# Kernel tuning notes

Hardware: AMD Instinct MI355X
Metric: run time of the kernel (lower is better)

Reference implementation:

```python
import jax, jax.numpy as jnp
import numpy as np

B, L, E, F = 4096, 200, 128, 64
NU = NI = 100000

def setup_inputs() -> dict:
    key = jax.random.key(0)
    ks = jax.random.split(key, 8)
    return {
        "user_ids": jax.random.randint(ks[0], (B,), 0, NU),
        "item_ids": jax.random.randint(ks[1], (B, L), 0, NI),
        "features": jax.random.normal(ks[2], (B, L, F), dtype=jnp.float32),
        "user_emb": jax.random.normal(ks[3], (NU, E), dtype=jnp.float32) * 0.1,
        "item_emb": jax.random.normal(ks[4], (NI, E), dtype=jnp.float32) * 0.1,
        "feat_w1": jax.random.normal(ks[5], (E, E + F), dtype=jnp.float32) * (2.0 / (E + F)) ** 0.5,
        "feat_b1": jnp.zeros((E,), jnp.float32),
        "feat_w2": jax.random.normal(ks[6], (E, E), dtype=jnp.float32) * (2.0 / E) ** 0.5,
        "feat_b2": jnp.zeros((E,), jnp.float32),
        "w1": jax.random.normal(ks[7], (E, 3 * E), dtype=jnp.float32) * (2.0 / (3 * E)) ** 0.5,
        "b1": jnp.zeros((E,), jnp.float32),
        "w2": jax.random.normal(jax.random.fold_in(key, 99), (1, E), dtype=jnp.float32) * (2.0 / E) ** 0.5,
        "b2": jnp.zeros((1,), jnp.float32),
    }

def reference(user_ids, item_ids, features, user_emb, item_emb,
              feat_w1, feat_b1, feat_w2, feat_b2, w1, b1, w2, b2):
    user = user_emb[user_ids]                      # [B, E]
    items = item_emb[item_ids]                     # [B, L, E]
    usern = jnp.broadcast_to(user[:, None, :], items.shape)  # [B, L, E]
    # FeatureNet: concat(user, features) -> Linear -> relu -> Linear -> relu
    fx = jnp.concatenate([usern, features], axis=-1)           # [B, L, E+F]
    fx = jax.nn.relu(jnp.einsum('blf,ef->ble', fx, feat_w1) + feat_b1)
    comp = jax.nn.relu(jnp.einsum('ble,oe->blo', fx, feat_w2) + feat_b2)  # [B, L, E]
    # attention MLP over concat(user, item, comp)
    x = jnp.concatenate([usern, items, comp], axis=-1)         # [B, L, 3E]
    x = jax.nn.relu(jnp.einsum('blf,ef->ble', x, w1) + b1)
    logits = jnp.einsum('ble,oe->blo', x, w2) + b2             # [B, L, 1]
    attn = jax.nn.softmax(logits, axis=1)                      # softmax over items
    out = user + jnp.sum(items * attn, axis=1)                 # [B, E]
    return out
```

## Files before the change

kernel.cpp:

```cpp
#include <hip/hip_runtime.h>
#include <math.h>

#define BB 4096
#define LL 200
#define EE 128
#define FF 64
#define NTHREADS 512

#define CROWS 32
#define NCH 7

#define PITCH_F  72
#define PITCH_FX 136
#define PITCH_X3 264

typedef __attribute__((ext_vector_type(4))) float  floatx4;
typedef __attribute__((ext_vector_type(8))) short  shortx8;

#define MFMA16(a, b, c) __builtin_amdgcn_mfma_f32_16x16x32_bf16((a), (b), (c), 0, 0, 0)

__device__ __forceinline__ unsigned cvt_pk_bf16(float lo, float hi) {
    unsigned r;
    asm("v_cvt_pk_bf16_f32 %0, %1, %2" : "=v"(r) : "v"(lo), "v"(hi));
    return r;
}
__device__ __forceinline__ unsigned short f2bf(float f) {
    return (unsigned short)cvt_pk_bf16(f, f);
}
__device__ __forceinline__ uint2 pk4(float4 v) {
    uint2 o;
    o.x = cvt_pk_bf16(v.x, v.y);
    o.y = cvt_pk_bf16(v.z, v.w);
    return o;
}

__device__ __forceinline__ shortx8 load_bfrag(const float* p) {
    float4 v0 = ((const float4*)p)[0];
    float4 v1 = ((const float4*)p)[1];
    union { unsigned u[4]; shortx8 s; } r;
    r.u[0] = cvt_pk_bf16(v0.x, v0.y);
    r.u[1] = cvt_pk_bf16(v0.z, v0.w);
    r.u[2] = cvt_pk_bf16(v1.x, v1.y);
    r.u[3] = cvt_pk_bf16(v1.z, v1.w);
    return r.s;
}

__device__ __forceinline__ float waveMax(float v) {
    #pragma unroll
    for (int off = 32; off > 0; off >>= 1)
        v = fmaxf(v, __shfl_xor(v, off, 64));
    return v;
}
__device__ __forceinline__ float waveSum(float v) {
    #pragma unroll
    for (int off = 32; off > 0; off >>= 1)
        v += __shfl_xor(v, off, 64);
    return v;
}

__global__ __launch_bounds__(NTHREADS, 4)
void usernet_mfma(const int* __restrict__ user_ids,
                  const int* __restrict__ item_ids,
                  const float* __restrict__ features,
                  const float* __restrict__ user_emb,
                  const float* __restrict__ item_emb,
                  const float* __restrict__ feat_w1,
                  const float* __restrict__ feat_b1,
                  const float* __restrict__ feat_w2,
                  const float* __restrict__ feat_b2,
                  const float* __restrict__ w1,
                  const float* __restrict__ b1,
                  const float* __restrict__ w2,
                  const float* __restrict__ b2,
                  float* __restrict__ out)
{
    __shared__ __align__(16) unsigned short s_feat[CROWS * PITCH_F];
    __shared__ __align__(16) unsigned short s_fx  [CROWS * PITCH_FX];
    __shared__ __align__(16) unsigned short s_x3  [CROWS * PITCH_X3];
    __shared__ float s_user[EE];
    __shared__ float s_bias1[EE];
    __shared__ float s_bias2[EE];
    __shared__ float s_bias3[EE];
    __shared__ float s_w2[EE];
    __shared__ float s_lp[8][CROWS];
    __shared__ float s_logit[208];
    __shared__ float s_attn[208];
    __shared__ float s_red[12];
    __shared__ float s_part[4][EE];

    const int b    = blockIdx.x;
    const int tid  = threadIdx.x;
    const int lane = tid & 63;
    const int wv   = tid >> 6;
    const int m    = lane & 15;
    const int q    = lane >> 4;
    const int n0   = wv * 16 + m;

    shortx8 B1[2];
    shortx8 B2[4];
    shortx8 B3[8];
    #pragma unroll
    for (int ks = 0; ks < 2; ++ks)
        B1[ks] = load_bfrag(feat_w1 + (size_t)n0 * (EE + FF) + EE + ks * 32 + q * 8);
    #pragma unroll
    for (int ks = 0; ks < 4; ++ks)
        B2[ks] = load_bfrag(feat_w2 + (size_t)n0 * EE + ks * 32 + q * 8);
    #pragma unroll
    for (int ks = 0; ks < 8; ++ks)
        B3[ks] = load_bfrag(w1 + (size_t)n0 * (3 * EE) + EE + ks * 32 + q * 8);

    if (tid < 32) {
        const int uid = user_ids[b];
        ((float4*)s_user)[tid] = ((const float4*)(user_emb + (size_t)uid * EE))[tid];
    }
    if (tid >= 64 && tid < 64 + EE) {
        s_bias2[tid - 64] = feat_b2[tid - 64];
        s_w2[tid - 64]    = w2[tid - 64];
    }
    __syncthreads();

    if (tid < 256) {
        const int e    = tid & (EE - 1);
        const int half = tid >> 7;
        const float* wrow = half ? (w1 + (size_t)e * (3 * EE))
                                 : (feat_w1 + (size_t)e * (EE + FF));
        float acc = 0.f;
        #pragma unroll 8
        for (int k = 0; k < EE; ++k) acc += wrow[k] * s_user[k];
        if (half == 0) s_bias1[e] = acc + feat_b1[e];
        else           s_bias3[e] = acc + b1[e];
    }
    __syncthreads();

    const float bias1_0 = s_bias1[n0];
    const float bias2_0 = s_bias2[n0];
    const float bias3_0 = s_bias3[n0];
    const float w2_0    = s_w2[n0];

    for (int ch = 0; ch < NCH; ++ch) {
        const int row0 = ch * CROWS;
        const int ntl  = (ch < NCH - 1) ? 2 : 1;
        const int rows = ntl * 16;

        if (ch > 0 && tid < CROWS) {
            float p = 0.f;
            #pragma unroll
            for (int w = 0; w < 8; ++w) p += s_lp[w][tid];
            s_logit[row0 - CROWS + tid] = p;
        }

        for (int idx = tid; idx < rows * 16; idx += NTHREADS) {
            const int r = idx >> 4, c4 = idx & 15;
            const int l = row0 + r;
            float4 v = make_float4(0.f, 0.f, 0.f, 0.f);
            if (l < LL) v = ((const float4*)features)[((size_t)b * LL + l) * 16 + c4];
            *(uint2*)&s_feat[r * PITCH_F + c4 * 4] = pk4(v);
        }
        for (int idx = tid; idx < rows * 32; idx += NTHREADS) {
            const int r = idx >> 5, c4 = idx & 31;
            const int l = row0 + r;
            float4 v = make_float4(0.f, 0.f, 0.f, 0.f);
            if (l < LL) {
                const int id = item_ids[(size_t)b * LL + l];
                v = ((const float4*)item_emb)[(size_t)id * 32 + c4];
            }
            *(uint2*)&s_x3[r * PITCH_X3 + c4 * 4] = pk4(v);
        }
        __syncthreads();

        for (int mt = 0; mt < ntl; ++mt) {
            floatx4 a0 = {0.f, 0.f, 0.f, 0.f};
            const unsigned short* ap = s_feat + (mt * 16 + m) * PITCH_F + q * 8;
            #pragma unroll
            for (int ks = 0; ks < 2; ++ks) {
                shortx8 af = *(const shortx8*)(ap + ks * 32);
                a0 = MFMA16(af, B1[ks], a0);
            }
            #pragma unroll
            for (int r = 0; r < 4; ++r) {
                const int row = mt * 16 + q * 4 + r;
                float v0 = a0[r] + bias1_0; v0 = v0 > 0.f ? v0 : 0.f;
                s_fx[row * PITCH_FX + n0] = f2bf(v0);
            }
        }
        __syncthreads();

        for (int mt = 0; mt < ntl; ++mt) {
            floatx4 a0 = {0.f, 0.f, 0.f, 0.f};
            const unsigned short* ap = s_fx + (mt * 16 + m) * PITCH_FX + q * 8;
            #pragma unroll
            for (int ks = 0; ks < 4; ++ks) {
                shortx8 af = *(const shortx8*)(ap + ks * 32);
                a0 = MFMA16(af, B2[ks], a0);
            }
            #pragma unroll
            for (int r = 0; r < 4; ++r) {
                const int row = mt * 16 + q * 4 + r;
                float v0 = a0[r] + bias2_0; v0 = v0 > 0.f ? v0 : 0.f;
                s_x3[row * PITCH_X3 + EE + n0] = f2bf(v0);
            }
        }
        __syncthreads();

        for (int mt = 0; mt < ntl; ++mt) {
            floatx4 a0 = {0.f, 0.f, 0.f, 0.f};
            const unsigned short* ap = s_x3 + (mt * 16 + m) * PITCH_X3 + q * 8;
            #pragma unroll
            for (int ks = 0; ks < 8; ++ks) {
                shortx8 af = *(const shortx8*)(ap + ks * 32);
                a0 = MFMA16(af, B3[ks], a0);
            }
            #pragma unroll
            for (int r = 0; r < 4; ++r) {
                float v0 = a0[r] + bias3_0; v0 = v0 > 0.f ? v0 : 0.f;
                float p = v0 * w2_0;
                p += __shfl_xor(p, 1, 64);
                p += __shfl_xor(p, 2, 64);
                p += __shfl_xor(p, 4, 64);
                p += __shfl_xor(p, 8, 64);
                if (m == 0) s_lp[wv][mt * 16 + q * 4 + r] = p;
            }
        }
        __syncthreads();
    }

    if (tid < 16) {
        float p = 0.f;
        #pragma unroll
        for (int w = 0; w < 8; ++w) p += s_lp[w][tid];
        s_logit[(NCH - 1) * CROWS + tid] = p;
    }
    __syncthreads();

    const int wid = tid >> 6;
    float lv = (tid < LL) ? s_logit[tid] : -INFINITY;
    {
        float mx = waveMax(lv);
        if ((tid & 63) == 0) s_red[wid] = mx;
        __syncthreads();
        if (tid == 0) {
            float g = s_red[0];
            #pragma unroll
            for (int w = 1; w < 8; ++w) g = fmaxf(g, s_red[w]);
            s_red[8] = g;
        }
        __syncthreads();
    }
    const float gmax = s_red[8];
    __syncthreads();
    float ex = (tid < LL) ? __expf(lv - gmax) : 0.f;
    {
        float s = waveSum(ex);
        if ((tid & 63) == 0) s_red[wid] = s;
        __syncthreads();
        if (tid == 0) {
            float g = 0.f;
            #pragma unroll
            for (int w = 0; w < 8; ++w) g += s_red[w];
            s_red[8] = g;
        }
        __syncthreads();
    }
    const float inv = 1.f / s_red[8];
    if (tid < LL) s_attn[tid] = ex * inv;
    __syncthreads();

    {
        const int e = tid & (EE - 1);
        const int g = tid >> 7;
        float acc = 0.f;
        const int lstart = g * (LL / 4);
        for (int l = lstart; l < lstart + LL / 4; ++l) {
            const float a  = s_attn[l];
            const int  id  = item_ids[(size_t)b * LL + l];
            acc += a * item_emb[(size_t)id * EE + e];
        }
        s_part[g][e] = acc;
        __syncthreads();
        if (tid < EE)
            out[(size_t)b * EE + tid] = s_user[tid] + s_part[0][tid] + s_part[1][tid]
                                      + s_part[2][tid] + s_part[3][tid];
    }
}

extern "C" void kernel_launch(void* const* d_in, const int* in_sizes, int n_in,
                              void* d_out, int out_size, void* d_ws, size_t ws_size,
                              hipStream_t stream) {
    const int*   user_ids = (const int*)  d_in[0];
    const int*   item_ids = (const int*)  d_in[1];
    const float* features = (const float*)d_in[2];
    const float* user_emb = (const float*)d_in[3];
    const float* item_emb = (const float*)d_in[4];
    const float* feat_w1  = (const float*)d_in[5];
    const float* feat_b1  = (const float*)d_in[6];
    const float* feat_w2  = (const float*)d_in[7];
    const float* feat_b2  = (const float*)d_in[8];
    const float* w1       = (const float*)d_in[9];
    const float* b1       = (const float*)d_in[10];
    const float* w2       = (const float*)d_in[11];
    const float* b2       = (const float*)d_in[12];
    float* out = (float*)d_out;

    usernet_mfma<<<BB, NTHREADS, 0, stream>>>(user_ids, item_ids, features,
                                              user_emb, item_emb,
                                              feat_w1, feat_b1, feat_w2, feat_b2,
                                              w1, b1, w2, b2, out);
}
```

Before: 747.6 us.

## Software-pipeline chunk gathers into registers with double-buffered item tiles

Issues the global loads for the next chunk's features and gathered item embeddings into registers at the start of each chunk, then writes them to shared memory after the current chunk's MFMA stages. Item tiles become double-buffered and the combined x3 buffer is split into item and comp buffers, which removes one barrier per chunk. The aim is to hide gather latency behind the MFMA work. In exchange it uses more registers and LDS, which could lower occupancy under the 4-blocks launch bound.

```diff
diff --git a/kernel.cpp b/kernel.cpp
--- a/kernel.cpp
+++ b/kernel.cpp
@@ -12,7 +12,6 @@
 
 #define PITCH_F  72
 #define PITCH_FX 136
-#define PITCH_X3 264
 
 typedef __attribute__((ext_vector_type(4))) float  floatx4;
 typedef __attribute__((ext_vector_type(8))) short  shortx8;
@@ -56,6 +55,57 @@
     for (int off = 32; off > 0; off >>= 1)
         v += __shfl_xor(v, off, 64);
     return v;
+}
+
+__device__ __forceinline__ void pf_load(int b, int row0n, int tid, bool en,
+                                        const float* __restrict__ features,
+                                        const int* __restrict__ item_ids,
+                                        const float* __restrict__ item_emb,
+                                        float4& f, float4& i0, float4& i1)
+{
+    f  = make_float4(0.f, 0.f, 0.f, 0.f);
+    i0 = make_float4(0.f, 0.f, 0.f, 0.f);
+    i1 = make_float4(0.f, 0.f, 0.f, 0.f);
+    if (!en) return;
+    {
+        const int r = tid >> 4, c4 = tid & 15, l = row0n + r;
+        if (l < LL) f = ((const float4*)features)[((size_t)b * LL + l) * 16 + c4];
+    }
+    {
+        const int r = tid >> 5, c4 = tid & 31, l = row0n + r;
+        if (l < LL) {
+            const int id = item_ids[(size_t)b * LL + l];
+            i0 = ((const float4*)item_emb)[(size_t)id * 32 + c4];
+        }
+    }
+    {
+        const int idx = tid + NTHREADS;
+        const int r = idx >> 5, c4 = idx & 31, l = row0n + r;
+        if (l < LL) {
+            const int id = item_ids[(size_t)b * LL + l];
+            i1 = ((const float4*)item_emb)[(size_t)id * 32 + c4];
+        }
+    }
+}
+
+__device__ __forceinline__ void pf_store(int tid, unsigned short* s_feat,
+                                         unsigned short* s_it_dst,
+                                         const float4& f, const float4& i0,
+                                         const float4& i1)
+{
+    {
+        const int r = tid >> 4, c4 = tid & 15;
+        *(uint2*)&s_feat[r * PITCH_F + c4 * 4] = pk4(f);
+    }
+    {
+        const int r = tid >> 5, c4 = tid & 31;
+        *(uint2*)&s_it_dst[r * PITCH_FX + c4 * 4] = pk4(i0);
+    }
+    {
+        const int idx = tid + NTHREADS;
+        const int r = idx >> 5, c4 = idx & 31;
+        *(uint2*)&s_it_dst[r * PITCH_FX + c4 * 4] = pk4(i1);
+    }
 }
 
 __global__ __launch_bounds__(NTHREADS, 4)
@@ -75,15 +125,16 @@
                   float* __restrict__ out)
 {
     __shared__ __align__(16) unsigned short s_feat[CROWS * PITCH_F];
+    __shared__ __align__(16) unsigned short s_it  [2][CROWS * PITCH_FX];
     __shared__ __align__(16) unsigned short s_fx  [CROWS * PITCH_FX];
-    __shared__ __align__(16) unsigned short s_x3  [CROWS * PITCH_X3];
+    __shared__ __align__(16) unsigned short s_comp[CROWS * PITCH_FX];
     __shared__ float s_user[EE];
     __shared__ float s_bias1[EE];
     __shared__ float s_bias2[EE];
     __shared__ float s_bias3[EE];
     __shared__ float s_w2[EE];
     __shared__ float s_lp[8][CROWS];
-    __shared__ float s_logit[208];
+    __shared__ float s_logit[224];
     __shared__ float s_attn[208];
     __shared__ float s_red[12];
     __shared__ float s_part[4][EE];
@@ -130,6 +181,10 @@
         if (half == 0) s_bias1[e] = acc + feat_b1[e];
         else           s_bias3[e] = acc + b1[e];
     }
+
+    float4 pf_f, pf_i0, pf_i1;
+    pf_load(b, 0, tid, true, features, item_ids, item_emb, pf_f, pf_i0, pf_i1);
+    pf_store(tid, s_feat, s_it[0], pf_f, pf_i0, pf_i1);
     __syncthreads();
 
     const float bias1_0 = s_bias1[n0];
@@ -140,7 +195,10 @@
     for (int ch = 0; ch < NCH; ++ch) {
         const int row0 = ch * CROWS;
         const int ntl  = (ch < NCH - 1) ? 2 : 1;
-        const int rows = ntl * 16;
+        const unsigned short* s_itc = s_it[ch & 1];
+
+        pf_load(b, (ch + 1) * CROWS, tid, ch + 1 < NCH,
+                features, item_ids, item_emb, pf_f, pf_i0, pf_i1);
 
         if (ch > 0 && tid < CROWS) {
             float p = 0.f;
@@ -148,25 +206,6 @@
             for (int w = 0; w < 8; ++w) p += s_lp[w][tid];
             s_logit[row0 - CROWS + tid] = p;
         }
-
-        for (int idx = tid; idx < rows * 16; idx += NTHREADS) {
-            const int r = idx >> 4, c4 = idx & 15;
-            const int l = row0 + r;
-            float4 v = make_float4(0.f, 0.f, 0.f, 0.f);
-            if (l < LL) v = ((const float4*)features)[((size_t)b * LL + l) * 16 + c4];
-            *(uint2*)&s_feat[r * PITCH_F + c4 * 4] = pk4(v);
-        }
-        for (int idx = tid; idx < rows * 32; idx += NTHREADS) {
-            const int r = idx >> 5, c4 = idx & 31;
-            const int l = row0 + r;
-            float4 v = make_float4(0.f, 0.f, 0.f, 0.f);
-            if (l < LL) {
-                const int id = item_ids[(size_t)b * LL + l];
-                v = ((const float4*)item_emb)[(size_t)id * 32 + c4];
-            }
-            *(uint2*)&s_x3[r * PITCH_X3 + c4 * 4] = pk4(v);
-        }
-        __syncthreads();
 
         for (int mt = 0; mt < ntl; ++mt) {
             floatx4 a0 = {0.f, 0.f, 0.f, 0.f};
@@ -197,18 +236,24 @@
             for (int r = 0; r < 4; ++r) {
                 const int row = mt * 16 + q * 4 + r;
                 float v0 = a0[r] + bias2_0; v0 = v0 > 0.f ? v0 : 0.f;
-                s_x3[row * PITCH_X3 + EE + n0] = f2bf(v0);
+                s_comp[row * PITCH_FX + n0] = f2bf(v0);
             }
         }
         __syncthreads();
 
         for (int mt = 0; mt < ntl; ++mt) {
             floatx4 a0 = {0.f, 0.f, 0.f, 0.f};
-            const unsigned short* ap = s_x3 + (mt * 16 + m) * PITCH_X3 + q * 8;
-            #pragma unroll
-            for (int ks = 0; ks < 8; ++ks) {
-                shortx8 af = *(const shortx8*)(ap + ks * 32);
+            const unsigned short* api = s_itc  + (mt * 16 + m) * PITCH_FX + q * 8;
+            const unsigned short* apc = s_comp + (mt * 16 + m) * PITCH_FX + q * 8;
+            #pragma unroll
+            for (int ks = 0; ks < 4; ++ks) {
+                shortx8 af = *(const shortx8*)(api + ks * 32);
                 a0 = MFMA16(af, B3[ks], a0);
+            }
+            #pragma unroll
+            for (int ks = 0; ks < 4; ++ks) {
+                shortx8 af = *(const shortx8*)(apc + ks * 32);
+                a0 = MFMA16(af, B3[4 + ks], a0);
             }
             #pragma unroll
             for (int r = 0; r < 4; ++r) {
@@ -221,6 +266,9 @@
                 if (m == 0) s_lp[wv][mt * 16 + q * 4 + r] = p;
             }
         }
+
+        if (ch + 1 < NCH)
+            pf_store(tid, s_feat, s_it[(ch + 1) & 1], pf_f, pf_i0, pf_i1);
         __syncthreads();
     }
 
```

Measured after the change: 701.0 us. 6.2% less time.
